# Kernel optimization log

Measured on AMD Instinct MI355X. Metric: run time of the kernel, lower is better.

The kernel has to match this reference:

```python
import jax, jax.numpy as jnp
import numpy as np

# Geometry / discretization constants (mirrors WaveCell.__init__)
NX, NY = 192, 192
DT = 1e-3
CMAX = 1.0
H = DT * CMAX * np.sqrt(2.0) * 1.01  # auto-set h as in __init__ (satisfies CFL)
SRC_X, SRC_Y = 96, 32  # point source grid location


def _laplacian(y, inv_h2):
    # y: [B, Nx, Ny]; 5-point stencil with zero padding (conv2d padding=1)
    p = jnp.pad(y, ((0, 0), (1, 1), (1, 1)))
    return inv_h2 * (p[:, :-2, 1:-1] + p[:, 2:, 1:-1]
                     + p[:, 1:-1, :-2] + p[:, 1:-1, 2:] - 4.0 * y)


def setup_inputs() -> dict:
    key = jax.random.key(0)
    k1, k2, k3 = jax.random.split(key, 3)
    B, T = 4, 256
    x = jax.random.normal(k1, (B, T, 1), dtype=jnp.float32)
    # per-cell wave speed in [0,1) so cmax <= 1 (CFL-safe)
    c = jax.random.uniform(k2, (NX, NY), dtype=jnp.float32)
    # boundary absorber damping coefficient
    b = jax.random.uniform(k3, (NX, NY), dtype=jnp.float32)
    return {"x": x, "c": c, "b": b}


def reference(x, c, b):
    B, T = x.shape[0], x.shape[1]
    inv_h2 = 1.0 / (H * H)
    inv_dt2 = 1.0 / (DT * DT)
    a_inv = 1.0 / (inv_dt2 + 0.5 * b / DT)   # [Nx, Ny]
    coef2 = inv_dt2 - 0.5 * b / DT           # [Nx, Ny]
    c2 = c * c

    x_seq = jnp.transpose(x[..., 0], (1, 0))  # [T, B]

    def step(carry, xt):
        y1, y2 = carry  # fields one and two steps ago
        y = a_inv * (2.0 * inv_dt2 * y1 - coef2 * y2 + c2 * _laplacian(y1, inv_h2))
        y = y.at[:, SRC_X, SRC_Y].add(xt)  # point source injection
        return (y, y1), y

    y0 = jnp.zeros((B, NX, NY), dtype=x.dtype)
    _, ys = jax.lax.scan(step, (y0, y0), x_seq)  # ys: [T, B, Nx, Ny]
    return jnp.transpose(ys, (1, 0, 2, 3))       # [B, T, Nx, Ny]
```

## Files before the change

### kernel.cpp

```cpp
#include <hip/hip_runtime.h>


#define NXg 192
#define NYg 192
#define BATCH 4
#define TSTEPS 256
#define CELLS (NXg * NYg)

#define TS 24
#define KSTEP 16
#define EXT 56
#define GROW 14
#define NP (EXT * GROW)
#define LROWS (EXT + 2)
#define LPITCH 64
#define LSZ (LROWS * LPITCH)
#define NTHREADS 512
#define NPT 2

#define SRC_X 96
#define SRC_Y 32

__global__ __launch_bounds__(NTHREADS) void wave_tile_kernel(
    const float* __restrict__ cg, const float* __restrict__ bg,
    const float* __restrict__ x, float* __restrict__ out, int t0) {
  __shared__ float buf0[LSZ];
  __shared__ float buf1[LSZ];

  const int tid = threadIdx.x;
  const int bcol = blockIdx.x;
  const int brow = blockIdx.y;
  const int bb = blockIdx.z;
  const int r0 = brow * TS - KSTEP;
  const int c0 = bcol * TS - KSTEP;
  const int obase = bb * TSTEPS * CELLS;
  const float inv_h2 = (float)(1.0 / (2.0 * 1.01 * 1.01 * 1.0e-3 * 1.0e-3));

  {
    float4 z = make_float4(0.f, 0.f, 0.f, 0.f);
    float4* p0 = (float4*)buf0;
    float4* p1 = (float4*)buf1;
    for (int i = tid; i < LSZ / 4; i += NTHREADS) {
      p0[i] = z;
      p1[i] = z;
    }
  }

  float xs[KSTEP];
  {
    const float4* xp = (const float4*)(x + bb * TSTEPS + t0);
    float4 a0 = xp[0], a1 = xp[1], a2 = xp[2], a3 = xp[3];
    xs[0] = a0.x; xs[1] = a0.y; xs[2] = a0.z; xs[3] = a0.w;
    xs[4] = a1.x; xs[5] = a1.y; xs[6] = a1.z; xs[7] = a1.w;
    xs[8] = a2.x; xs[9] = a2.y; xs[10] = a2.z; xs[11] = a2.w;
    xs[12] = a3.x; xs[13] = a3.y; xs[14] = a3.z; xs[15] = a3.w;
  }

  float4 yc[NPT], yp[NPT], ai[NPT], cf[NPT], cs[NPT], sm[NPT];
  int loff[NPT], gofs[NPT];
  bool act[NPT], til[NPT];

#pragma unroll
  for (int it = 0; it < NPT; ++it) {
    const int p = tid + it * NTHREADS;
    const float4 z = make_float4(0.f, 0.f, 0.f, 0.f);
    yc[it] = z; yp[it] = z; ai[it] = z; cf[it] = z; cs[it] = z; sm[it] = z;
    loff[it] = LPITCH + 4; gofs[it] = 0; til[it] = false;
    act[it] = (p < NP);
    if (act[it]) {
      const int lr = p / GROW;
      const int lg = p % GROW;
      loff[it] = (lr + 1) * LPITCH + 4 + lg * 4;
      const int gr = r0 + lr;
      const int gc = c0 + lg * 4;
      til[it] = (lr >= KSTEP && lr < KSTEP + TS && lg >= 4 && lg < 10);
      if (gr >= 0 && gr < NXg && gc >= 0 && gc < NYg) {
        const int gi = gr * NYg + gc;
        gofs[it] = gi;
        float4 cv = *(const float4*)(cg + gi);
        float4 bv = *(const float4*)(bg + gi);
        ai[it].x = 1.0f / (1.0e6f + 500.0f * bv.x);
        ai[it].y = 1.0f / (1.0e6f + 500.0f * bv.y);
        ai[it].z = 1.0f / (1.0e6f + 500.0f * bv.z);
        ai[it].w = 1.0f / (1.0e6f + 500.0f * bv.w);
        cf[it].x = 1.0e6f - 500.0f * bv.x;
        cf[it].y = 1.0e6f - 500.0f * bv.y;
        cf[it].z = 1.0e6f - 500.0f * bv.z;
        cf[it].w = 1.0e6f - 500.0f * bv.w;
        cs[it].x = cv.x * cv.x;
        cs[it].y = cv.y * cv.y;
        cs[it].z = cv.z * cv.z;
        cs[it].w = cv.w * cv.w;
        if (t0 > 0) {
          yc[it] = *(const float4*)(out + obase + (t0 - 1) * CELLS + gi);
          yp[it] = *(const float4*)(out + obase + (t0 - 2) * CELLS + gi);
        }
        if (gr == SRC_X && SRC_Y >= gc && SRC_Y < gc + 4) {
          ((float*)&sm[it])[SRC_Y - gc] = 1.0f;
        }
      }
    }
  }

  __syncthreads();

#pragma unroll
  for (int it = 0; it < NPT; ++it) {
    if (act[it]) *(float4*)&buf0[loff[it]] = yc[it];
  }
  __syncthreads();

  float* ping = buf0;
  float* pong = buf1;

#pragma unroll
  for (int j = 0; j < KSTEP; ++j) {
    const float xt = xs[j];
    float* op = out + obase + (t0 + j) * CELLS;
#pragma unroll
    for (int it = 0; it < NPT; ++it) {
      if (act[it]) {
        const int lo = loff[it];
        float4 up = *(float4*)&ping[lo - LPITCH];
        float4 dn = *(float4*)&ping[lo + LPITCH];
        float4 lq = *(float4*)&ping[lo - 4];
        float4 rq = *(float4*)&ping[lo + 4];
        float4 v1 = yc[it];
        float4 vp = yp[it];
        float4 av = ai[it], fv = cf[it], sv = cs[it], smv = sm[it];
        float4 val;
        {
          float lap = inv_h2 * (up.x + dn.x + lq.w + v1.y - 4.0f * v1.x);
          val.x = av.x * (2.0e6f * v1.x - fv.x * vp.x + sv.x * lap) + smv.x * xt;
        }
        {
          float lap = inv_h2 * (up.y + dn.y + v1.x + v1.z - 4.0f * v1.y);
          val.y = av.y * (2.0e6f * v1.y - fv.y * vp.y + sv.y * lap) + smv.y * xt;
        }
        {
          float lap = inv_h2 * (up.z + dn.z + v1.y + v1.w - 4.0f * v1.z);
          val.z = av.z * (2.0e6f * v1.z - fv.z * vp.z + sv.z * lap) + smv.z * xt;
        }
        {
          float lap = inv_h2 * (up.w + dn.w + v1.z + rq.x - 4.0f * v1.w);
          val.w = av.w * (2.0e6f * v1.w - fv.w * vp.w + sv.w * lap) + smv.w * xt;
        }
        yp[it] = v1;
        yc[it] = val;
        *(float4*)&pong[lo] = val;
        if (til[it]) *(float4*)(op + gofs[it]) = val;
      }
    }
    __syncthreads();
    float* tmp = ping; ping = pong; pong = tmp;
  }
}

extern "C" void kernel_launch(void* const* d_in, const int* in_sizes, int n_in,
                              void* d_out, int out_size, void* d_ws,
                              size_t ws_size, hipStream_t stream) {
  const float* x = (const float*)d_in[0];
  const float* c = (const float*)d_in[1];
  const float* b = (const float*)d_in[2];
  float* out = (float*)d_out;

  dim3 grid(NXg / TS, NYg / TS, BATCH);
  for (int t0 = 0; t0 < TSTEPS; t0 += KSTEP) {
    wave_tile_kernel<<<grid, NTHREADS, 0, stream>>>(c, b, x, out, t0);
  }
}
```

Baseline: 367.5 us.

## Give each thread 8 columns and use wave shuffles for horizontal neighbors

Each thread now owns one row segment of 8 cells (two float4s) instead of two separate 4-cell segments, using 448 threads where the 8th lane of each row is padding. Left and right neighbor values come from lane shuffles rather than shared-memory loads, and the LDS pitch is changed to 68 to reduce bank conflicts on the vertical loads. This cuts LDS traffic per cell and removes the per-item loop and predicates. In exchange, one lane in eight does no useful work.

```diff
diff --git a/kernel.cpp b/kernel.cpp
--- a/kernel.cpp
+++ b/kernel.cpp
@@ -10,24 +10,23 @@
 #define TS 24
 #define KSTEP 16
 #define EXT 56
-#define GROW 14
-#define NP (EXT * GROW)
 #define LROWS (EXT + 2)
-#define LPITCH 64
+#define LPITCH 68
 #define LSZ (LROWS * LPITCH)
-#define NTHREADS 512
-#define NPT 2
+#define NTHREADS 448
 
 #define SRC_X 96
 #define SRC_Y 32
 
 __global__ __launch_bounds__(NTHREADS) void wave_tile_kernel(
-    const float* __restrict__ cg, const float* __restrict__ bg,
+    const float* __restrict__ cgp, const float* __restrict__ bgp,
     const float* __restrict__ x, float* __restrict__ out, int t0) {
   __shared__ float buf0[LSZ];
   __shared__ float buf1[LSZ];
 
   const int tid = threadIdx.x;
+  const int lr = tid >> 3;
+  const int lg = tid & 7;
   const int bcol = blockIdx.x;
   const int brow = blockIdx.y;
   const int bb = blockIdx.z;
@@ -56,58 +55,66 @@
     xs[12] = a3.x; xs[13] = a3.y; xs[14] = a3.z; xs[15] = a3.w;
   }
 
-  float4 yc[NPT], yp[NPT], ai[NPT], cf[NPT], cs[NPT], sm[NPT];
-  int loff[NPT], gofs[NPT];
-  bool act[NPT], til[NPT];
+  const int lo = (lr + 1) * LPITCH + 4 + 8 * lg;
 
-#pragma unroll
-  for (int it = 0; it < NPT; ++it) {
-    const int p = tid + it * NTHREADS;
-    const float4 z = make_float4(0.f, 0.f, 0.f, 0.f);
-    yc[it] = z; yp[it] = z; ai[it] = z; cf[it] = z; cs[it] = z; sm[it] = z;
-    loff[it] = LPITCH + 4; gofs[it] = 0; til[it] = false;
-    act[it] = (p < NP);
-    if (act[it]) {
-      const int lr = p / GROW;
-      const int lg = p % GROW;
-      loff[it] = (lr + 1) * LPITCH + 4 + lg * 4;
-      const int gr = r0 + lr;
-      const int gc = c0 + lg * 4;
-      til[it] = (lr >= KSTEP && lr < KSTEP + TS && lg >= 4 && lg < 10);
-      if (gr >= 0 && gr < NXg && gc >= 0 && gc < NYg) {
-        const int gi = gr * NYg + gc;
-        gofs[it] = gi;
-        float4 cv = *(const float4*)(cg + gi);
-        float4 bv = *(const float4*)(bg + gi);
-        ai[it].x = 1.0f / (1.0e6f + 500.0f * bv.x);
-        ai[it].y = 1.0f / (1.0e6f + 500.0f * bv.y);
-        ai[it].z = 1.0f / (1.0e6f + 500.0f * bv.z);
-        ai[it].w = 1.0f / (1.0e6f + 500.0f * bv.w);
-        cf[it].x = 1.0e6f - 500.0f * bv.x;
-        cf[it].y = 1.0e6f - 500.0f * bv.y;
-        cf[it].z = 1.0e6f - 500.0f * bv.z;
-        cf[it].w = 1.0e6f - 500.0f * bv.w;
-        cs[it].x = cv.x * cv.x;
-        cs[it].y = cv.y * cv.y;
-        cs[it].z = cv.z * cv.z;
-        cs[it].w = cv.w * cv.w;
-        if (t0 > 0) {
-          yc[it] = *(const float4*)(out + obase + (t0 - 1) * CELLS + gi);
-          yp[it] = *(const float4*)(out + obase + (t0 - 2) * CELLS + gi);
-        }
-        if (gr == SRC_X && SRC_Y >= gc && SRC_Y < gc + 4) {
-          ((float*)&sm[it])[SRC_Y - gc] = 1.0f;
-        }
-      }
+  const int gr = r0 + lr;
+  const int gc = c0 + 8 * lg;
+  const bool id = (lg < 7) && (gr >= 0) && (gr < NXg) && (gc >= 0) && (gc < NYg);
+  const bool til = (lr >= KSTEP) && (lr < KSTEP + TS) && (lg >= 2) && (lg < 5);
+  const int gofs = id ? (gr * NYg + gc) : 0;
+
+  const float4 z4 = make_float4(0.f, 0.f, 0.f, 0.f);
+  float4 yc0 = z4, yc1 = z4, yp0 = z4, yp1 = z4;
+  float4 ai0 = z4, ai1 = z4, cf0 = z4, cf1 = z4, cs0 = z4, cs1 = z4;
+  float4 sm0 = z4, sm1 = z4;
+
+  if (id) {
+    float4 cv0 = *(const float4*)(cgp + gofs);
+    float4 cv1 = *(const float4*)(cgp + gofs + 4);
+    float4 bv0 = *(const float4*)(bgp + gofs);
+    float4 bv1 = *(const float4*)(bgp + gofs + 4);
+    ai0.x = 1.0f / (1.0e6f + 500.0f * bv0.x);
+    ai0.y = 1.0f / (1.0e6f + 500.0f * bv0.y);
+    ai0.z = 1.0f / (1.0e6f + 500.0f * bv0.z);
+    ai0.w = 1.0f / (1.0e6f + 500.0f * bv0.w);
+    ai1.x = 1.0f / (1.0e6f + 500.0f * bv1.x);
+    ai1.y = 1.0f / (1.0e6f + 500.0f * bv1.y);
+    ai1.z = 1.0f / (1.0e6f + 500.0f * bv1.z);
+    ai1.w = 1.0f / (1.0e6f + 500.0f * bv1.w);
+    cf0.x = 1.0e6f - 500.0f * bv0.x;
+    cf0.y = 1.0e6f - 500.0f * bv0.y;
+    cf0.z = 1.0e6f - 500.0f * bv0.z;
+    cf0.w = 1.0e6f - 500.0f * bv0.w;
+    cf1.x = 1.0e6f - 500.0f * bv1.x;
+    cf1.y = 1.0e6f - 500.0f * bv1.y;
+    cf1.z = 1.0e6f - 500.0f * bv1.z;
+    cf1.w = 1.0e6f - 500.0f * bv1.w;
+    cs0.x = cv0.x * cv0.x; cs0.y = cv0.y * cv0.y;
+    cs0.z = cv0.z * cv0.z; cs0.w = cv0.w * cv0.w;
+    cs1.x = cv1.x * cv1.x; cs1.y = cv1.y * cv1.y;
+    cs1.z = cv1.z * cv1.z; cs1.w = cv1.w * cv1.w;
+    if (t0 > 0) {
+      yc0 = *(const float4*)(out + obase + (t0 - 1) * CELLS + gofs);
+      yc1 = *(const float4*)(out + obase + (t0 - 1) * CELLS + gofs + 4);
+      yp0 = *(const float4*)(out + obase + (t0 - 2) * CELLS + gofs);
+      yp1 = *(const float4*)(out + obase + (t0 - 2) * CELLS + gofs + 4);
+    }
+    if (gr == SRC_X) {
+      sm0.x = (gc + 0 == SRC_Y) ? 1.0f : 0.0f;
+      sm0.y = (gc + 1 == SRC_Y) ? 1.0f : 0.0f;
+      sm0.z = (gc + 2 == SRC_Y) ? 1.0f : 0.0f;
+      sm0.w = (gc + 3 == SRC_Y) ? 1.0f : 0.0f;
+      sm1.x = (gc + 4 == SRC_Y) ? 1.0f : 0.0f;
+      sm1.y = (gc + 5 == SRC_Y) ? 1.0f : 0.0f;
+      sm1.z = (gc + 6 == SRC_Y) ? 1.0f : 0.0f;
+      sm1.w = (gc + 7 == SRC_Y) ? 1.0f : 0.0f;
     }
   }
 
   __syncthreads();
 
-#pragma unroll
-  for (int it = 0; it < NPT; ++it) {
-    if (act[it]) *(float4*)&buf0[loff[it]] = yc[it];
-  }
+  *(float4*)&buf0[lo] = yc0;
+  *(float4*)&buf0[lo + 4] = yc1;
   __syncthreads();
 
   float* ping = buf0;
@@ -117,40 +124,61 @@
   for (int j = 0; j < KSTEP; ++j) {
     const float xt = xs[j];
     float* op = out + obase + (t0 + j) * CELLS;
-#pragma unroll
-    for (int it = 0; it < NPT; ++it) {
-      if (act[it]) {
-        const int lo = loff[it];
-        float4 up = *(float4*)&ping[lo - LPITCH];
-        float4 dn = *(float4*)&ping[lo + LPITCH];
-        float4 lq = *(float4*)&ping[lo - 4];
-        float4 rq = *(float4*)&ping[lo + 4];
-        float4 v1 = yc[it];
-        float4 vp = yp[it];
-        float4 av = ai[it], fv = cf[it], sv = cs[it], smv = sm[it];
-        float4 val;
-        {
-          float lap = inv_h2 * (up.x + dn.x + lq.w + v1.y - 4.0f * v1.x);
-          val.x = av.x * (2.0e6f * v1.x - fv.x * vp.x + sv.x * lap) + smv.x * xt;
-        }
-        {
-          float lap = inv_h2 * (up.y + dn.y + v1.x + v1.z - 4.0f * v1.y);
-          val.y = av.y * (2.0e6f * v1.y - fv.y * vp.y + sv.y * lap) + smv.y * xt;
-        }
-        {
-          float lap = inv_h2 * (up.z + dn.z + v1.y + v1.w - 4.0f * v1.z);
-          val.z = av.z * (2.0e6f * v1.z - fv.z * vp.z + sv.z * lap) + smv.z * xt;
-        }
-        {
-          float lap = inv_h2 * (up.w + dn.w + v1.z + rq.x - 4.0f * v1.w);
-          val.w = av.w * (2.0e6f * v1.w - fv.w * vp.w + sv.w * lap) + smv.w * xt;
-        }
-        yp[it] = v1;
-        yc[it] = val;
-        *(float4*)&pong[lo] = val;
-        if (til[it]) *(float4*)(op + gofs[it]) = val;
-      }
+
+    float lqw = __shfl_up(yc1.w, 1);
+    lqw = (lg == 0) ? 0.0f : lqw;
+    float rqx = __shfl_down(yc0.x, 1);
+
+    float4 up0 = *(float4*)&ping[lo - LPITCH];
+    float4 up1 = *(float4*)&ping[lo - LPITCH + 4];
+    float4 dn0 = *(float4*)&ping[lo + LPITCH];
+    float4 dn1 = *(float4*)&ping[lo + LPITCH + 4];
+
+    float4 val0, val1;
+    {
+      float lap = inv_h2 * (up0.x + dn0.x + lqw + yc0.y - 4.0f * yc0.x);
+      val0.x = ai0.x * (2.0e6f * yc0.x - cf0.x * yp0.x + cs0.x * lap) + sm0.x * xt;
     }
+    {
+      float lap = inv_h2 * (up0.y + dn0.y + yc0.x + yc0.z - 4.0f * yc0.y);
+      val0.y = ai0.y * (2.0e6f * yc0.y - cf0.y * yp0.y + cs0.y * lap) + sm0.y * xt;
+    }
+    {
+      float lap = inv_h2 * (up0.z + dn0.z + yc0.y + yc0.w - 4.0f * yc0.z);
+      val0.z = ai0.z * (2.0e6f * yc0.z - cf0.z * yp0.z + cs0.z * lap) + sm0.z * xt;
+    }
+    {
+      float lap = inv_h2 * (up0.w + dn0.w + yc0.z + yc1.x - 4.0f * yc0.w);
+      val0.w = ai0.w * (2.0e6f * yc0.w - cf0.w * yp0.w + cs0.w * lap) + sm0.w * xt;
+    }
+    {
+      float lap = inv_h2 * (up1.x + dn1.x + yc0.w + yc1.y - 4.0f * yc1.x);
+      val1.x = ai1.x * (2.0e6f * yc1.x - cf1.x * yp1.x + cs1.x * lap) + sm1.x * xt;
+    }
+    {
+      float lap = inv_h2 * (up1.y + dn1.y + yc1.x + yc1.z - 4.0f * yc1.y);
+      val1.y = ai1.y * (2.0e6f * yc1.y - cf1.y * yp1.y + cs1.y * lap) + sm1.y * xt;
+    }
+    {
+      float lap = inv_h2 * (up1.z + dn1.z + yc1.y + yc1.w - 4.0f * yc1.z);
+      val1.z = ai1.z * (2.0e6f * yc1.z - cf1.z * yp1.z + cs1.z * lap) + sm1.z * xt;
+    }
+    {
+      float lap = inv_h2 * (up1.w + dn1.w + yc1.z + rqx - 4.0f * yc1.w);
+      val1.w = ai1.w * (2.0e6f * yc1.w - cf1.w * yp1.w + cs1.w * lap) + sm1.w * xt;
+    }
+
+    yp0 = yc0; yp1 = yc1;
+    yc0 = val0; yc1 = val1;
+
+    *(float4*)&pong[lo] = val0;
+    *(float4*)&pong[lo + 4] = val1;
+
+    if (til) {
+      *(float4*)(op + gofs) = val0;
+      *(float4*)(op + gofs + 4) = val1;
+    }
+
     __syncthreads();
     float* tmp = ping; ping = pong; pong = tmp;
   }
```

New measurement: 327.2 us. 11.0% less time.
